# Kernel tuning notes

Measured on AMD Instinct MI355X. Metric: run time of the kernel, lower is better.

Reference implementation:

```python
import jax, jax.numpy as jnp
import numpy as np

B, N, D = 32, 512, 256
ITERATION_STEPS = 2


def setup_inputs() -> dict:
    key = jax.random.key(0)
    ks = jax.random.split(key, 20)
    node = jax.random.normal(ks[0], (B, N, D), dtype=jnp.float32)
    node_mask = jnp.ones((B, N), dtype=jnp.int32)
    graphs = [(jax.random.uniform(ks[1 + i], (B, N, N)) < 0.05).astype(jnp.int32)
              for i in range(6)]
    s = 0.02
    params = {
        'w_nw': jax.random.normal(ks[8], (D, 1)) * s,
        'b_nw': jnp.zeros((1,), jnp.float32),
        'w_self': jax.random.normal(ks[9], (D, D)) * s,
        'b_self': jnp.zeros((D,), jnp.float32),
        'w_arg1': jax.random.normal(ks[10], (D, D)) * s,
        'w_arg2': jax.random.normal(ks[11], (D, D)) * s,
        'w_arg3': jax.random.normal(ks[12], (D, D)) * s,
        'w_arg4': jax.random.normal(ks[13], (D, D)) * s,
        'w_punct': jax.random.normal(ks[14], (D, D)) * s,
        'w_punct_re': jax.random.normal(ks[15], (D, D)) * s,
    }
    return {'node': node, 'node_mask': node_mask,
            'arg_graph_1': graphs[0], 'arg_graph_2': graphs[1],
            'arg_graph_3': graphs[2], 'arg_graph_4': graphs[3],
            'punct_graph': graphs[4], 'punct_graph_re': graphs[5],
            **params}


def reference(node, node_mask, arg_graph_1, arg_graph_2, arg_graph_3, arg_graph_4,
              punct_graph, punct_graph_re,
              w_nw, b_nw, w_self, b_self,
              w_arg1, w_arg2, w_arg3, w_arg4, w_punct, w_punct_re):
    n = node.shape[1]
    diag = jnp.eye(n, dtype=node_mask.dtype)  # [N,N]
    # dd_graph: pairwise valid mask with zeroed diagonal, [B,N,N]
    dd = node_mask[:, None, :] * node_mask[:, :, None] * (1 - diag)
    G = jnp.stack([arg_graph_1, arg_graph_2, arg_graph_3, arg_graph_4,
                   punct_graph, punct_graph_re], 0) * dd[None]  # [6,B,N,N]
    Gf = G.astype(node.dtype)
    # neighbor count over all 6 edge types; replace 0 by 1 to avoid div-by-zero
    nn_num = Gf.sum(axis=(0, -1))  # [B,N]
    nn_num = jnp.where(nn_num >= 1, nn_num, jnp.ones_like(nn_num))
    W = jnp.stack([w_arg1, w_arg2, w_arg3, w_arg4, w_punct, w_punct_re], 0)  # [6,D,D]

    all_weight = []
    for _ in range(ITERATION_STEPS):
        # (1) node relatedness measure
        d_node_weight = jax.nn.sigmoid(node @ w_nw + b_nw)[..., 0]  # [B,N]
        all_weight.append(d_node_weight)
        self_node_info = node @ w_self + b_self  # [B,N,D]
        # (2) message propagation: per edge type k, project then aggregate
        proj = jnp.einsum('bnd,kde->kbne', node, W)            # [6,B,N,D]
        masked_w = d_node_weight[None, :, None, :] * Gf        # [6,B,N,N]
        agg = jnp.einsum('kbmn,kbne->bme', masked_w, proj)     # [B,N,D]
        # (3) update
        node = jax.nn.relu(self_node_info + agg / nn_num[..., None])
    return node, jnp.stack(all_weight, axis=1)  # [B,N,D], [B,steps,N]
```

## Files before the change

### kernel.cpp

```cpp
#include <hip/hip_runtime.h>

#define Bb 32
#define Nn 512
#define Dd 256
#define KC 1792
#define NR (Bb * Nn)

typedef __bf16 bf16x8 __attribute__((ext_vector_type(8)));
typedef float  f32x4  __attribute__((ext_vector_type(4)));
typedef int    i32x4  __attribute__((ext_vector_type(4)));
typedef unsigned short u16;

__device__ __forceinline__ u16 f2bf(float x){
  union { float f; unsigned u; } c; c.f = x;
  unsigned u = c.u;
  u += 0x7FFFu + ((u >> 16) & 1u);
  return (u16)(u >> 16);
}

__global__ __launch_bounds__(256) void k_prep(
    const float* __restrict__ wself,
    const float* __restrict__ w0, const float* __restrict__ w1,
    const float* __restrict__ w2, const float* __restrict__ w3,
    const float* __restrict__ w4, const float* __restrict__ w5,
    u16* __restrict__ wcatT){
  int e = blockIdx.x;
  const float* Ws[7] = {wself, w0, w1, w2, w3, w4, w5};
  for (int c = threadIdx.x; c < KC; c += 256){
    int g = c >> 8, j = c & 255;
    wcatT[(size_t)e*KC + c] = f2bf(Ws[g][j*Dd + e]);
  }
}

#define GLD(d, p, o) asm volatile("global_load_dwordx4 %0, %1, off offset:" #o \
                                  : "=v"(d) : "v"(p))

__global__ __launch_bounds__(256) void k_pack(
    const int* __restrict__ g0, const int* __restrict__ g1,
    const int* __restrict__ g2, const int* __restrict__ g3,
    const int* __restrict__ g4, const int* __restrict__ g5,
    const int* __restrict__ mask,
    unsigned* __restrict__ Gp, float* __restrict__ rs){
  int t = threadIdx.x, l = t & 63, wv = t >> 6;
  int r = blockIdx.x * 4 + wv;
  int b = r >> 9, m = r & 511;
  size_t off = (size_t)r * Nn + l * 4;
  const int* pm = mask + (size_t)b * Nn + l * 4;
  const int* pa = g0 + off; const int* pb = g1 + off; const int* pcx = g2 + off;
  const int* pd = g3 + off; const int* pe = g4 + off; const int* pf = g5 + off;

  i32x4 A0,A1,B0,B1,C0,C1,D0,D1,E0,E1,F0,F1,M0,M1;
  GLD(M0,pm,0);  GLD(M1,pm,1024);
  GLD(A0,pa,0);  GLD(A1,pa,1024);
  GLD(B0,pb,0);  GLD(B1,pb,1024);
  GLD(C0,pcx,0); GLD(C1,pcx,1024);
  GLD(D0,pd,0);  GLD(D1,pd,1024);
  GLD(E0,pe,0);  GLD(E1,pe,1024);
  GLD(F0,pf,0);  GLD(F1,pf,1024);
  asm volatile("s_waitcnt vmcnt(0)" ::: "memory");
  __builtin_amdgcn_sched_barrier(0);

  int s1 = (l & 1) * 4, s2 = ((l >> 1) & 1) * 8, s3 = ((l >> 2) & 1) * 16;
  unsigned dm0 = ((m >> 2) == l)      ? (1u << (m & 3)) : 0u;
  unsigned dm1 = ((m >> 2) == 64 + l) ? (1u << (m & 3)) : 0u;
  int stot = 0;
#define PK(G, MM, DM, k, h) {                                              \
    unsigned nib = (unsigned)((G[0] & MM[0]) | ((G[1] & MM[1]) << 1) |     \
                              ((G[2] & MM[2]) << 2) | ((G[3] & MM[3]) << 3)) \
                   & ~(DM);                                                \
    stot += __popc(nib);                                                   \
    unsigned v = nib << s1; v |= (unsigned)__shfl_xor((int)v, 1);          \
    v <<= s2;               v |= (unsigned)__shfl_xor((int)v, 2);          \
    v <<= s3;               v |= (unsigned)__shfl_xor((int)v, 4);          \
    if ((l & 7) == 0)                                                      \
      Gp[((size_t)(k) * NR + r) * 16 + (h) * 8 + (l >> 3)] = v; }
  PK(A0,M0,dm0,0,0) PK(A1,M1,dm1,0,1)
  PK(B0,M0,dm0,1,0) PK(B1,M1,dm1,1,1)
  PK(C0,M0,dm0,2,0) PK(C1,M1,dm1,2,1)
  PK(D0,M0,dm0,3,0) PK(D1,M1,dm1,3,1)
  PK(E0,M0,dm0,4,0) PK(E1,M1,dm1,4,1)
  PK(F0,M0,dm0,5,0) PK(F1,M1,dm1,5,1)
#undef PK
  #pragma unroll
  for (int o = 1; o < 64; o <<= 1) stot += __shfl_xor(stot, o);
  if (l == 0)
    rs[r] = mask[r] ? 1.0f / (float)(stot < 1 ? 1 : stot) : 0.0f;
}
#undef GLD

__global__ __launch_bounds__(256) void k_dw(
    const float* __restrict__ node, const int* __restrict__ mask,
    const float* __restrict__ wnw, const float* __restrict__ bnw,
    float* __restrict__ aw_out,
    u16* __restrict__ Z, u16* __restrict__ XT){
  __shared__ float tile[32][268];
  __shared__ float dws[32];
  int b = blockIdx.x >> 4, n0 = (blockIdx.x & 15) << 5;
  int t = threadIdx.x;
  int row = t >> 3, seg = t & 7;
  const float* src = node + ((size_t)(b * Nn + n0 + row)) * Dd + seg * 32;
  u16* zn = Z + ((size_t)(b * Nn + n0 + row)) * KC + seg * 32;
  #pragma unroll
  for (int c = 0; c < 8; ++c){
    float4 v = ((const float4*)src)[c];
    tile[row][seg * 32 + c * 4 + 0] = v.x;
    tile[row][seg * 32 + c * 4 + 1] = v.y;
    tile[row][seg * 32 + c * 4 + 2] = v.z;
    tile[row][seg * 32 + c * 4 + 3] = v.w;
    ushort4 h;
    h.x = f2bf(v.x); h.y = f2bf(v.y); h.z = f2bf(v.z); h.w = f2bf(v.w);
    ((ushort4*)zn)[c] = h;
  }
  __syncthreads();
  float s = 0.f;
  #pragma unroll
  for (int c = 0; c < 32; ++c) s += tile[row][seg * 32 + c] * wnw[seg * 32 + c];
  s += __shfl_xor(s, 1); s += __shfl_xor(s, 2); s += __shfl_xor(s, 4);
  if (seg == 0){
    float dw = 1.f / (1.f + expf(-(s + bnw[0])));
    aw_out[b * (2 * Nn) + n0 + row] = dw;
    dws[row] = mask[b * Nn + n0 + row] ? dw : 0.f;
  }
  __syncthreads();
  #pragma unroll
  for (int p = 0; p < 4; ++p){
    int d = p * 64 + (t >> 2);
    int j0 = (t & 3) * 8;
    union { u16 h[8]; uint4 v; } pk;
    #pragma unroll
    for (int jj = 0; jj < 8; ++jj)
      pk.h[jj] = f2bf(dws[j0 + jj] * tile[j0 + jj][d]);
    *(uint4*)(XT + ((size_t)(b * Dd + d)) * Nn + n0 + j0) = pk.v;
  }
}

__global__ __launch_bounds__(256) void k_agg(
    const unsigned* __restrict__ Gp,
    const u16* __restrict__ XT, const float* __restrict__ rs,
    u16* __restrict__ Z){
  int mt = blockIdx.x, b = blockIdx.y, kg = blockIdx.z;
  int m0 = mt * 64;
  const unsigned* Gr = Gp + ((size_t)kg * Bb * Nn + b * Nn + m0) * 16;
  const u16* Xb = XT + (size_t)b * Dd * Nn;
  __shared__ u16 As[64 * 72];
  __shared__ u16 Bs[256 * 72];
  int t = threadIdx.x, lane = t & 63, wn = t >> 6;
  int arow = t >> 2, aq = t & 3;
  unsigned wpre[8];
  #pragma unroll
  for (int ks = 0; ks < 8; ++ks)
    wpre[ks] = Gr[arow * 16 + ks * 2 + (aq >> 1)];

  f32x4 acc[4][4];
  #pragma unroll
  for (int i = 0; i < 4; ++i)
    #pragma unroll
    for (int q = 0; q < 4; ++q) acc[i][q] = (f32x4){0.f, 0.f, 0.f, 0.f};

  for (int ks = 0; ks < 8; ++ks){
    int k0 = ks * 64;
    {
      unsigned bits = (wpre[ks] >> ((aq & 1) * 16)) & 0xFFFFu;
      union { u16 h[16]; uint4 v[2]; } pk;
      #pragma unroll
      for (int c = 0; c < 16; ++c)
        pk.h[c] = ((bits >> c) & 1u) ? 0x3F80 : 0;
      *(uint4*)&As[arow * 72 + aq * 16]     = pk.v[0];
      *(uint4*)&As[arow * 72 + aq * 16 + 8] = pk.v[1];
    }
    #pragma unroll
    for (int p = 0; p < 8; ++p){
      int rowb = p * 32 + (t >> 3);
      *(uint4*)&Bs[rowb * 72 + (t & 7) * 8] =
          *(const uint4*)(Xb + (size_t)rowb * Nn + k0 + (t & 7) * 8);
    }
    __syncthreads();
    #pragma unroll
    for (int kk = 0; kk < 2; ++kk){
      bf16x8 av[4], bv[4];
      #pragma unroll
      for (int i = 0; i < 4; ++i)
        av[i] = *(const bf16x8*)&As[(i * 16 + (lane & 15)) * 72 + kk * 32 + (lane >> 4) * 8];
      #pragma unroll
      for (int q = 0; q < 4; ++q)
        bv[q] = *(const bf16x8*)&Bs[(wn * 64 + q * 16 + (lane & 15)) * 72 + kk * 32 + (lane >> 4) * 8];
      #pragma unroll
      for (int i = 0; i < 4; ++i)
        #pragma unroll
        for (int q = 0; q < 4; ++q)
          acc[i][q] = __builtin_amdgcn_mfma_f32_16x16x32_bf16(av[i], bv[q], acc[i][q], 0, 0, 0);
    }
    __syncthreads();
  }
  int kgcol = 256 + kg * 256 + wn * 64;
  #pragma unroll
  for (int i = 0; i < 4; ++i){
    #pragma unroll
    for (int r = 0; r < 4; ++r){
      int mg = m0 + i * 16 + (lane >> 4) * 4 + r;
      float sc = rs[b * Nn + mg];
      u16* zp = Z + ((size_t)(b * Nn + mg)) * KC + kgcol + (lane & 15);
      #pragma unroll
      for (int q = 0; q < 4; ++q)
        zp[q * 16] = f2bf(acc[i][q][r] * sc);
    }
  }
}

__global__ __launch_bounds__(256) void k_upd(
    const u16* __restrict__ Z, const u16* __restrict__ wcatT,
    const float* __restrict__ bself, float* __restrict__ outp){
  int n0 = blockIdx.x * 128, m0 = blockIdx.y * 128;
  __shared__ u16 As[128 * 72];
  __shared__ u16 Bs[128 * 72];
  int t = threadIdx.x, lane = t & 63, wid = t >> 6;
  int wm = wid >> 1, wn = wid & 1;
  f32x4 acc[4][4];
  #pragma unroll
  for (int i = 0; i < 4; ++i)
    #pragma unroll
    for (int q = 0; q < 4; ++q) acc[i][q] = (f32x4){0.f, 0.f, 0.f, 0.f};

  for (int ks = 0; ks < 28; ++ks){
    int k0 = ks * 64;
    #pragma unroll
    for (int p = 0; p < 4; ++p){
      int row = p * 32 + (t >> 3);
      *(uint4*)&As[row * 72 + (t & 7) * 8] =
          *(const uint4*)(Z + ((size_t)(m0 + row)) * KC + k0 + (t & 7) * 8);
      *(uint4*)&Bs[row * 72 + (t & 7) * 8] =
          *(const uint4*)(wcatT + ((size_t)(n0 + row)) * KC + k0 + (t & 7) * 8);
    }
    __syncthreads();
    #pragma unroll
    for (int kk = 0; kk < 2; ++kk){
      bf16x8 av[4], bv[4];
      #pragma unroll
      for (int i = 0; i < 4; ++i)
        av[i] = *(const bf16x8*)&As[(wm * 64 + i * 16 + (lane & 15)) * 72 + kk * 32 + (lane >> 4) * 8];
      #pragma unroll
      for (int q = 0; q < 4; ++q)
        bv[q] = *(const bf16x8*)&Bs[(wn * 64 + q * 16 + (lane & 15)) * 72 + kk * 32 + (lane >> 4) * 8];
      #pragma unroll
      for (int i = 0; i < 4; ++i)
        #pragma unroll
        for (int q = 0; q < 4; ++q)
          acc[i][q] = __builtin_amdgcn_mfma_f32_16x16x32_bf16(av[i], bv[q], acc[i][q], 0, 0, 0);
    }
    __syncthreads();
  }
  #pragma unroll
  for (int i = 0; i < 4; ++i){
    #pragma unroll
    for (int r = 0; r < 4; ++r){
      int mg = m0 + wm * 64 + i * 16 + (lane >> 4) * 4 + r;
      #pragma unroll
      for (int q = 0; q < 4; ++q){
        int e = n0 + wn * 64 + q * 16 + (lane & 15);
        float v = acc[i][q][r] + bself[e];
        outp[(size_t)mg * Dd + e] = v > 0.f ? v : 0.f;
      }
    }
  }
}

extern "C" void kernel_launch(void* const* d_in, const int* in_sizes, int n_in,
                              void* d_out, int out_size, void* d_ws, size_t ws_size,
                              hipStream_t stream){
  (void)in_sizes; (void)n_in; (void)out_size; (void)ws_size;
  const float* node  = (const float*)d_in[0];
  const int*   mask  = (const int*)d_in[1];
  const int*   g[6];
  for (int i = 0; i < 6; ++i) g[i] = (const int*)d_in[2 + i];
  const float* wnw   = (const float*)d_in[8];
  const float* bnw   = (const float*)d_in[9];
  const float* wself = (const float*)d_in[10];
  const float* bself = (const float*)d_in[11];
  const float* W[6];
  for (int i = 0; i < 6; ++i) W[i] = (const float*)d_in[12 + i];

  float* out_node = (float*)d_out;
  float* out_aw   = out_node + (size_t)Bb * Nn * Dd;

  char* ws = (char*)d_ws;
  u16*      wcatT = (u16*)(ws);
  float*    rs    = (float*)(ws + 917504);
  unsigned* Gp    = (unsigned*)(ws + 1048576);
  u16*      XT    = (u16*)(ws + 7340032);
  u16*      Z     = (u16*)(ws + 15728640);

  k_prep<<<256, 256, 0, stream>>>(wself, W[0], W[1], W[2], W[3], W[4], W[5], wcatT);
  k_pack<<<4096, 256, 0, stream>>>(g[0], g[1], g[2], g[3], g[4], g[5], mask, Gp, rs);

  for (int t = 0; t < 2; ++t){
    const float* nsrc = (t == 0) ? node : out_node;
    k_dw<<<512, 256, 0, stream>>>(nsrc, mask, wnw, bnw, out_aw + t * Nn, Z, XT);
    k_agg<<<dim3(8, 32, 6), 256, 0, stream>>>(Gp, XT, rs, Z);
    k_upd<<<dim3(2, 128), 256, 0, stream>>>(Z, wcatT, bself, out_node);
  }
}
```

Baseline: 245.6 us.

## Fuse aggregation and update GEMMs into one kernel, dropping Z intermediate

Merges the per-edge-type aggregation GEMM and the final projection GEMM into one kernel. Each block computes the aggregated tile for each edge type into shared memory, then immediately multiplies it by the corresponding weight slice into a persistent output accumulator. This removes the global write and read of the wide concatenated Z buffer and one launch per iteration. In exchange the grid shrinks to 256 blocks with heavy shared memory use and serialized per-type work, reducing parallelism and occupancy.

```diff
diff --git a/kernel.cpp b/kernel.cpp
--- a/kernel.cpp
+++ b/kernel.cpp
@@ -92,14 +92,14 @@
     const float* __restrict__ node, const int* __restrict__ mask,
     const float* __restrict__ wnw, const float* __restrict__ bnw,
     float* __restrict__ aw_out,
-    u16* __restrict__ Z, u16* __restrict__ XT){
+    u16* __restrict__ Nbf, u16* __restrict__ XT){
   __shared__ float tile[32][268];
   __shared__ float dws[32];
   int b = blockIdx.x >> 4, n0 = (blockIdx.x & 15) << 5;
   int t = threadIdx.x;
   int row = t >> 3, seg = t & 7;
   const float* src = node + ((size_t)(b * Nn + n0 + row)) * Dd + seg * 32;
-  u16* zn = Z + ((size_t)(b * Nn + n0 + row)) * KC + seg * 32;
+  u16* zn = Nbf + ((size_t)(b * Nn + n0 + row)) * Dd + seg * 32;
   #pragma unroll
   for (int c = 0; c < 8; ++c){
     float4 v = ((const float4*)src)[c];
@@ -134,131 +134,138 @@
   }
 }
 
-__global__ __launch_bounds__(256) void k_agg(
-    const unsigned* __restrict__ Gp,
-    const u16* __restrict__ XT, const float* __restrict__ rs,
-    u16* __restrict__ Z){
-  int mt = blockIdx.x, b = blockIdx.y, kg = blockIdx.z;
-  int m0 = mt * 64;
-  const unsigned* Gr = Gp + ((size_t)kg * Bb * Nn + b * Nn + m0) * 16;
-  const u16* Xb = XT + (size_t)b * Dd * Nn;
+__global__ __launch_bounds__(256, 1) void k_fuse(
+    const unsigned* __restrict__ Gp, const u16* __restrict__ XT,
+    const u16* __restrict__ Nbf, const u16* __restrict__ wcatT,
+    const float* __restrict__ rs, const float* __restrict__ bself,
+    float* __restrict__ outp){
   __shared__ u16 As[64 * 72];
-  __shared__ u16 Bs[256 * 72];
+  __shared__ u16 BW[256 * 72];
+  __shared__ u16 Ts[64 * 264];
+  int mt = blockIdx.x, b = blockIdx.y, m0 = mt * 64;
   int t = threadIdx.x, lane = t & 63, wn = t >> 6;
   int arow = t >> 2, aq = t & 3;
-  unsigned wpre[8];
-  #pragma unroll
-  for (int ks = 0; ks < 8; ++ks)
-    wpre[ks] = Gr[arow * 16 + ks * 2 + (aq >> 1)];
-
-  f32x4 acc[4][4];
+  const u16* Xb = XT + (size_t)b * Dd * Nn;
+
+  float rsv[16];
   #pragma unroll
   for (int i = 0; i < 4; ++i)
     #pragma unroll
-    for (int q = 0; q < 4; ++q) acc[i][q] = (f32x4){0.f, 0.f, 0.f, 0.f};
-
-  for (int ks = 0; ks < 8; ++ks){
-    int k0 = ks * 64;
-    {
-      unsigned bits = (wpre[ks] >> ((aq & 1) * 16)) & 0xFFFFu;
-      union { u16 h[16]; uint4 v[2]; } pk;
-      #pragma unroll
-      for (int c = 0; c < 16; ++c)
-        pk.h[c] = ((bits >> c) & 1u) ? 0x3F80 : 0;
-      *(uint4*)&As[arow * 72 + aq * 16]     = pk.v[0];
-      *(uint4*)&As[arow * 72 + aq * 16 + 8] = pk.v[1];
+    for (int r = 0; r < 4; ++r)
+      rsv[i * 4 + r] = rs[b * Nn + m0 + i * 16 + (lane >> 4) * 4 + r];
+
+  f32x4 accO[4][4];
+  #pragma unroll
+  for (int i = 0; i < 4; ++i)
+    #pragma unroll
+    for (int q = 0; q < 4; ++q) accO[i][q] = (f32x4){0.f, 0.f, 0.f, 0.f};
+
+  for (int k = 0; k < 7; ++k){
+    if (k < 6){
+      const unsigned* Gr = Gp + ((size_t)k * NR + b * Nn + m0) * 16;
+      unsigned wpre[8];
+      #pragma unroll
+      for (int ks = 0; ks < 8; ++ks)
+        wpre[ks] = Gr[arow * 16 + ks * 2 + (aq >> 1)];
+      f32x4 Ta[4][4];
+      #pragma unroll
+      for (int i = 0; i < 4; ++i)
+        #pragma unroll
+        for (int q = 0; q < 4; ++q) Ta[i][q] = (f32x4){0.f, 0.f, 0.f, 0.f};
+
+      for (int ks = 0; ks < 8; ++ks){
+        int k0 = ks * 64;
+        {
+          unsigned bits = (wpre[ks] >> ((aq & 1) * 16)) & 0xFFFFu;
+          union { u16 h[16]; uint4 v[2]; } pk;
+          #pragma unroll
+          for (int c = 0; c < 16; ++c)
+            pk.h[c] = ((bits >> c) & 1u) ? 0x3F80 : 0;
+          *(uint4*)&As[arow * 72 + aq * 16]     = pk.v[0];
+          *(uint4*)&As[arow * 72 + aq * 16 + 8] = pk.v[1];
+        }
+        #pragma unroll
+        for (int p = 0; p < 8; ++p){
+          int rowb = p * 32 + (t >> 3);
+          *(uint4*)&BW[rowb * 72 + (t & 7) * 8] =
+              *(const uint4*)(Xb + (size_t)rowb * Nn + k0 + (t & 7) * 8);
+        }
+        __syncthreads();
+        #pragma unroll
+        for (int kk = 0; kk < 2; ++kk){
+          bf16x8 av[4], bv[4];
+          #pragma unroll
+          for (int i = 0; i < 4; ++i)
+            av[i] = *(const bf16x8*)&As[(i * 16 + (lane & 15)) * 72 + kk * 32 + (lane >> 4) * 8];
+          #pragma unroll
+          for (int q = 0; q < 4; ++q)
+            bv[q] = *(const bf16x8*)&BW[(wn * 64 + q * 16 + (lane & 15)) * 72 + kk * 32 + (lane >> 4) * 8];
+          #pragma unroll
+          for (int i = 0; i < 4; ++i)
+            #pragma unroll
+            for (int q = 0; q < 4; ++q)
+              Ta[i][q] = __builtin_amdgcn_mfma_f32_16x16x32_bf16(av[i], bv[q], Ta[i][q], 0, 0, 0);
+        }
+        __syncthreads();
+      }
+      #pragma unroll
+      for (int i = 0; i < 4; ++i)
+        #pragma unroll
+        for (int r = 0; r < 4; ++r){
+          int row = i * 16 + (lane >> 4) * 4 + r;
+          #pragma unroll
+          for (int q = 0; q < 4; ++q)
+            Ts[row * 264 + wn * 64 + q * 16 + (lane & 15)] =
+                f2bf(Ta[i][q][r] * rsv[i * 4 + r]);
+        }
+      __syncthreads();
+    } else {
+      const u16* Nb = Nbf + ((size_t)(b * Nn + m0)) * Dd;
+      #pragma unroll
+      for (int p = 0; p < 8; ++p){
+        int row = p * 8 + (t >> 5), col = (t & 31) * 8;
+        *(uint4*)&Ts[row * 264 + col] = *(const uint4*)(Nb + (size_t)row * Dd + col);
+      }
+      __syncthreads();
     }
-    #pragma unroll
-    for (int p = 0; p < 8; ++p){
-      int rowb = p * 32 + (t >> 3);
-      *(uint4*)&Bs[rowb * 72 + (t & 7) * 8] =
-          *(const uint4*)(Xb + (size_t)rowb * Nn + k0 + (t & 7) * 8);
+    int cb = (k < 6) ? (256 + k * 256) : 0;
+    for (int cs = 0; cs < 4; ++cs){
+      int c0 = cs * 64;
+      #pragma unroll
+      for (int p = 0; p < 8; ++p){
+        int rowb = p * 32 + (t >> 3);
+        *(uint4*)&BW[rowb * 72 + (t & 7) * 8] =
+            *(const uint4*)(wcatT + (size_t)rowb * KC + cb + c0 + (t & 7) * 8);
+      }
+      __syncthreads();
+      #pragma unroll
+      for (int kk = 0; kk < 2; ++kk){
+        bf16x8 av[4], bv[4];
+        #pragma unroll
+        for (int i = 0; i < 4; ++i)
+          av[i] = *(const bf16x8*)&Ts[(i * 16 + (lane & 15)) * 264 + c0 + kk * 32 + (lane >> 4) * 8];
+        #pragma unroll
+        for (int q = 0; q < 4; ++q)
+          bv[q] = *(const bf16x8*)&BW[(wn * 64 + q * 16 + (lane & 15)) * 72 + kk * 32 + (lane >> 4) * 8];
+        #pragma unroll
+        for (int i = 0; i < 4; ++i)
+          #pragma unroll
+          for (int q = 0; q < 4; ++q)
+            accO[i][q] = __builtin_amdgcn_mfma_f32_16x16x32_bf16(av[i], bv[q], accO[i][q], 0, 0, 0);
+      }
+      __syncthreads();
     }
-    __syncthreads();
-    #pragma unroll
-    for (int kk = 0; kk < 2; ++kk){
-      bf16x8 av[4], bv[4];
-      #pragma unroll
-      for (int i = 0; i < 4; ++i)
-        av[i] = *(const bf16x8*)&As[(i * 16 + (lane & 15)) * 72 + kk * 32 + (lane >> 4) * 8];
-      #pragma unroll
-      for (int q = 0; q < 4; ++q)
-        bv[q] = *(const bf16x8*)&Bs[(wn * 64 + q * 16 + (lane & 15)) * 72 + kk * 32 + (lane >> 4) * 8];
-      #pragma unroll
-      for (int i = 0; i < 4; ++i)
-        #pragma unroll
-        for (int q = 0; q < 4; ++q)
-          acc[i][q] = __builtin_amdgcn_mfma_f32_16x16x32_bf16(av[i], bv[q], acc[i][q], 0, 0, 0);
-    }
-    __syncthreads();
-  }
-  int kgcol = 256 + kg * 256 + wn * 64;
+  }
   #pragma unroll
   for (int i = 0; i < 4; ++i){
     #pragma unroll
     for (int r = 0; r < 4; ++r){
-      int mg = m0 + i * 16 + (lane >> 4) * 4 + r;
-      float sc = rs[b * Nn + mg];
-      u16* zp = Z + ((size_t)(b * Nn + mg)) * KC + kgcol + (lane & 15);
-      #pragma unroll
-      for (int q = 0; q < 4; ++q)
-        zp[q * 16] = f2bf(acc[i][q][r] * sc);
-    }
-  }
-}
-
-__global__ __launch_bounds__(256) void k_upd(
-    const u16* __restrict__ Z, const u16* __restrict__ wcatT,
-    const float* __restrict__ bself, float* __restrict__ outp){
-  int n0 = blockIdx.x * 128, m0 = blockIdx.y * 128;
-  __shared__ u16 As[128 * 72];
-  __shared__ u16 Bs[128 * 72];
-  int t = threadIdx.x, lane = t & 63, wid = t >> 6;
-  int wm = wid >> 1, wn = wid & 1;
-  f32x4 acc[4][4];
-  #pragma unroll
-  for (int i = 0; i < 4; ++i)
-    #pragma unroll
-    for (int q = 0; q < 4; ++q) acc[i][q] = (f32x4){0.f, 0.f, 0.f, 0.f};
-
-  for (int ks = 0; ks < 28; ++ks){
-    int k0 = ks * 64;
-    #pragma unroll
-    for (int p = 0; p < 4; ++p){
-      int row = p * 32 + (t >> 3);
-      *(uint4*)&As[row * 72 + (t & 7) * 8] =
-          *(const uint4*)(Z + ((size_t)(m0 + row)) * KC + k0 + (t & 7) * 8);
-      *(uint4*)&Bs[row * 72 + (t & 7) * 8] =
-          *(const uint4*)(wcatT + ((size_t)(n0 + row)) * KC + k0 + (t & 7) * 8);
-    }
-    __syncthreads();
-    #pragma unroll
-    for (int kk = 0; kk < 2; ++kk){
-      bf16x8 av[4], bv[4];
-      #pragma unroll
-      for (int i = 0; i < 4; ++i)
-        av[i] = *(const bf16x8*)&As[(wm * 64 + i * 16 + (lane & 15)) * 72 + kk * 32 + (lane >> 4) * 8];
-      #pragma unroll
-      for (int q = 0; q < 4; ++q)
-        bv[q] = *(const bf16x8*)&Bs[(wn * 64 + q * 16 + (lane & 15)) * 72 + kk * 32 + (lane >> 4) * 8];
-      #pragma unroll
-      for (int i = 0; i < 4; ++i)
-        #pragma unroll
-        for (int q = 0; q < 4; ++q)
-          acc[i][q] = __builtin_amdgcn_mfma_f32_16x16x32_bf16(av[i], bv[q], acc[i][q], 0, 0, 0);
-    }
-    __syncthreads();
-  }
-  #pragma unroll
-  for (int i = 0; i < 4; ++i){
-    #pragma unroll
-    for (int r = 0; r < 4; ++r){
-      int mg = m0 + wm * 64 + i * 16 + (lane >> 4) * 4 + r;
+      size_t gr = (size_t)b * Nn + m0 + i * 16 + (lane >> 4) * 4 + r;
       #pragma unroll
       for (int q = 0; q < 4; ++q){
-        int e = n0 + wn * 64 + q * 16 + (lane & 15);
-        float v = acc[i][q][r] + bself[e];
-        outp[(size_t)mg * Dd + e] = v > 0.f ? v : 0.f;
+        int e = wn * 64 + q * 16 + (lane & 15);
+        float v = accO[i][q][r] + bself[e];
+        outp[gr * Dd + e] = v > 0.f ? v : 0.f;
       }
     }
   }
@@ -287,15 +294,14 @@
   float*    rs    = (float*)(ws + 917504);
   unsigned* Gp    = (unsigned*)(ws + 1048576);
   u16*      XT    = (u16*)(ws + 7340032);
-  u16*      Z     = (u16*)(ws + 15728640);
+  u16*      Nbf   = (u16*)(ws + 15728640);
 
   k_prep<<<256, 256, 0, stream>>>(wself, W[0], W[1], W[2], W[3], W[4], W[5], wcatT);
   k_pack<<<4096, 256, 0, stream>>>(g[0], g[1], g[2], g[3], g[4], g[5], mask, Gp, rs);
 
   for (int t = 0; t < 2; ++t){
     const float* nsrc = (t == 0) ? node : out_node;
-    k_dw<<<512, 256, 0, stream>>>(nsrc, mask, wnw, bnw, out_aw + t * Nn, Z, XT);
-    k_agg<<<dim3(8, 32, 6), 256, 0, stream>>>(Gp, XT, rs, Z);
-    k_upd<<<dim3(2, 128), 256, 0, stream>>>(Z, wcatT, bself, out_node);
-  }
-}
+    k_dw<<<512, 256, 0, stream>>>(nsrc, mask, wnw, bnw, out_aw + t * Nn, Nbf, XT);
+    k_fuse<<<dim3(8, 32), 256, 0, stream>>>(Gp, XT, Nbf, wcatT, rs, bself, out_node);
+  }
+}
```

New measurement: 260.2 us. 1.06x slower.
